# Kernel tuning notes

Measured on AMD Instinct MI355X. Metric: run time of the kernel, lower is better.

Reference implementation:

```python
import jax, jax.numpy as jnp
import numpy as np

EPS = 1e-6
NUM_SEMANTICS = 8
HIDDEN = 768
BATCH = 4096


def _gram_schmidt_single(vectors, fallback):
    """Sequential (classical, per-torch-code) Gram-Schmidt on (S, D) vectors.
    fallback: (S, D) random vectors used when a residual norm falls below EPS.
    """
    S = vectors.shape[0]
    qs = []
    for i in range(S):
        v = vectors[i]
        for j in range(i):
            qj = qs[j]
            denom = jnp.dot(qj, qj)
            safe_denom = jnp.where(denom > 0, denom, 1.0)
            proj = jnp.dot(v, qj) / safe_denom
            # torch: only subtract if ||q_j|| > eps
            v = jnp.where(jnp.sqrt(denom) > EPS, v - proj * qj, v)
        norm = jnp.linalg.norm(v)
        safe_norm = jnp.where(norm > 0, norm, 1.0)
        fb = fallback[i]
        fb = fb / jnp.linalg.norm(fb)
        q = jnp.where(norm > EPS, v / safe_norm, fb)
        qs.append(q)
    return jnp.stack(qs, axis=0)


def setup_inputs() -> dict:
    key = jax.random.key(0)
    semantic_reprs = jax.random.normal(key, (BATCH, NUM_SEMANTICS, HIDDEN), dtype=jnp.float32)
    return {"semantic_reprs": semantic_reprs}


def reference(semantic_reprs):
    B, S, D = semantic_reprs.shape
    # fixed fallback random vectors (stand-in for torch.randn_like in the degenerate branch)
    fallback = jax.random.normal(jax.random.key(42), (B, S, D), dtype=semantic_reprs.dtype)
    return jax.vmap(_gram_schmidt_single)(semantic_reprs, fallback)
```

## Files before the change

### kernel.cpp

```cpp
#include <hip/hip_runtime.h>


#define S_VECS 8
#define D_DIM 768
#define CHUNKS 192

typedef float f32x4 __attribute__((ext_vector_type(4)));

__device__ __forceinline__ float wave_reduce_sum(float x) {
#pragma unroll
    for (int off = 32; off >= 1; off >>= 1)
        x += __shfl_xor(x, off, 64);
    return x;
}

__global__ __launch_bounds__(192)
void gram_schmidt_kernel(const float* __restrict__ in, float* __restrict__ out) {
    const int wave = threadIdx.x >> 6;
    const int lane = threadIdx.x & 63;
    const int b = blockIdx.x;
    const int chunk = wave * 64 + lane;

    __shared__ float red[2][S_VECS][3];

    const int w1 = (wave == 2) ? 0 : wave + 1;
    const int w2 = (wave == 0) ? 2 : wave - 1;

    float v[S_VECS][4];
    const f32x4* src = reinterpret_cast<const f32x4*>(in) + (size_t)b * (S_VECS * CHUNKS);
#pragma unroll
    for (int s = 0; s < S_VECS; ++s) {
        f32x4 f = src[s * CHUNKS + chunk];
        v[s][0] = f.x; v[s][1] = f.y; v[s][2] = f.z; v[s][3] = f.w;
    }

    float inv_n[S_VECS];

#pragma unroll
    for (int i = 1; i < S_VECS; ++i) {
        const int p = i & 1;
        float d[S_VECS];
#pragma unroll
        for (int j = 0; j < S_VECS; ++j) {
            if (j < i) {
                float acc = 0.f;
#pragma unroll
                for (int e = 0; e < 4; ++e) acc += v[i][e] * v[j][e];
                d[j] = acc;
            }
        }
        float self = 0.f;
#pragma unroll
        for (int e = 0; e < 4; ++e) self += v[i - 1][e] * v[i - 1][e];

#pragma unroll
        for (int j = 0; j < S_VECS; ++j) {
            if (j < i) d[j] = wave_reduce_sum(d[j]);
        }
        self = wave_reduce_sum(self);

        if (lane == 0) {
#pragma unroll
            for (int j = 0; j < S_VECS; ++j) {
                if (j < i) red[p][j][wave] = d[j];
            }
            red[p][i][wave] = self;
        }
        __syncthreads();
#pragma unroll
        for (int j = 0; j < S_VECS; ++j) {
            if (j < i) d[j] += red[p][j][w1] + red[p][j][w2];
        }
        self += red[p][i][w1] + red[p][i][w2];
        inv_n[i - 1] = 1.0f / self;

#pragma unroll
        for (int j = 0; j < S_VECS; ++j) {
            if (j < i) {
                const float proj = d[j] * inv_n[j];
#pragma unroll
                for (int e = 0; e < 4; ++e) v[i][e] -= proj * v[j][e];
            }
        }
    }

    {
        float self = 0.f;
#pragma unroll
        for (int e = 0; e < 4; ++e) self += v[S_VECS - 1][e] * v[S_VECS - 1][e];
        self = wave_reduce_sum(self);
        if (lane == 0) red[0][0][wave] = self;
        __syncthreads();
        self += red[0][0][w1] + red[0][0][w2];
        inv_n[S_VECS - 1] = 1.0f / self;
    }

    f32x4* dst = reinterpret_cast<f32x4*>(out) + (size_t)b * (S_VECS * CHUNKS);
#pragma unroll
    for (int s = 0; s < S_VECS; ++s) {
        const float inv_norm = sqrtf(inv_n[s]);
        f32x4 f;
        f.x = v[s][0] * inv_norm;
        f.y = v[s][1] * inv_norm;
        f.z = v[s][2] * inv_norm;
        f.w = v[s][3] * inv_norm;
        __builtin_nontemporal_store(f, &dst[s * CHUNKS + chunk]);
    }
}

extern "C" void kernel_launch(void* const* d_in, const int* in_sizes, int n_in,
                              void* d_out, int out_size, void* d_ws, size_t ws_size,
                              hipStream_t stream) {
    const float* in = (const float*)d_in[0];
    float* out = (float*)d_out;
    const int B = in_sizes[0] / (S_VECS * D_DIM);
    gram_schmidt_kernel<<<B, 192, 0, stream>>>(in, out);
}
```

Before: 42.50 us.

## Replace sequential Gram-Schmidt with Gram matrix Cholesky and triangular inverse

Instead of projecting one vector at a time with a block barrier per step, the kernel computes the full 36-entry upper Gram matrix in one pass, reduces it across waves with a single barrier, and then runs a Cholesky factorisation redundantly in every thread. It inverts the triangular factor and forms the orthonormal outputs as linear combinations of the original vectors. This removes seven serialized reduce/sync rounds, in exchange for more wave shuffles at once, higher register pressure, and the numerical-stability and degenerate-case differences of Cholesky QR.

```diff
diff --git a/kernel.cpp b/kernel.cpp
--- a/kernel.cpp
+++ b/kernel.cpp
@@ -1,9 +1,9 @@
 #include <hip/hip_runtime.h>
 
 
-#define S_VECS 8
-#define D_DIM 768
+#define S 8
 #define CHUNKS 192
+#define IDX(i, j) ((i)*S - ((i) * ((i) + 1)) / 2 + (j))
 
 typedef float f32x4 __attribute__((ext_vector_type(4)));
 
@@ -15,95 +15,117 @@
 }
 
 __global__ __launch_bounds__(192)
-void gram_schmidt_kernel(const float* __restrict__ in, float* __restrict__ out) {
+void gs_chol_kernel(const float* __restrict__ in, float* __restrict__ out) {
     const int wave = threadIdx.x >> 6;
     const int lane = threadIdx.x & 63;
     const int b = blockIdx.x;
     const int chunk = wave * 64 + lane;
 
-    __shared__ float red[2][S_VECS][3];
+    __shared__ __align__(16) float red[3][36];
 
-    const int w1 = (wave == 2) ? 0 : wave + 1;
-    const int w2 = (wave == 0) ? 2 : wave - 1;
-
-    float v[S_VECS][4];
-    const f32x4* src = reinterpret_cast<const f32x4*>(in) + (size_t)b * (S_VECS * CHUNKS);
+    float v[S][4];
+    const f32x4* src = reinterpret_cast<const f32x4*>(in) + (size_t)b * (S * CHUNKS);
 #pragma unroll
-    for (int s = 0; s < S_VECS; ++s) {
+    for (int s = 0; s < S; ++s) {
         f32x4 f = src[s * CHUNKS + chunk];
         v[s][0] = f.x; v[s][1] = f.y; v[s][2] = f.z; v[s][3] = f.w;
     }
 
-    float inv_n[S_VECS];
-
+    float d[36];
 #pragma unroll
-    for (int i = 1; i < S_VECS; ++i) {
-        const int p = i & 1;
-        float d[S_VECS];
+    for (int i = 0; i < S; ++i) {
 #pragma unroll
-        for (int j = 0; j < S_VECS; ++j) {
-            if (j < i) {
+        for (int j = 0; j < S; ++j) {
+            if (j >= i) {
                 float acc = 0.f;
 #pragma unroll
                 for (int e = 0; e < 4; ++e) acc += v[i][e] * v[j][e];
-                d[j] = acc;
-            }
-        }
-        float self = 0.f;
-#pragma unroll
-        for (int e = 0; e < 4; ++e) self += v[i - 1][e] * v[i - 1][e];
-
-#pragma unroll
-        for (int j = 0; j < S_VECS; ++j) {
-            if (j < i) d[j] = wave_reduce_sum(d[j]);
-        }
-        self = wave_reduce_sum(self);
-
-        if (lane == 0) {
-#pragma unroll
-            for (int j = 0; j < S_VECS; ++j) {
-                if (j < i) red[p][j][wave] = d[j];
-            }
-            red[p][i][wave] = self;
-        }
-        __syncthreads();
-#pragma unroll
-        for (int j = 0; j < S_VECS; ++j) {
-            if (j < i) d[j] += red[p][j][w1] + red[p][j][w2];
-        }
-        self += red[p][i][w1] + red[p][i][w2];
-        inv_n[i - 1] = 1.0f / self;
-
-#pragma unroll
-        for (int j = 0; j < S_VECS; ++j) {
-            if (j < i) {
-                const float proj = d[j] * inv_n[j];
-#pragma unroll
-                for (int e = 0; e < 4; ++e) v[i][e] -= proj * v[j][e];
+                d[IDX(i, j)] = acc;
             }
         }
     }
 
-    {
-        float self = 0.f;
 #pragma unroll
-        for (int e = 0; e < 4; ++e) self += v[S_VECS - 1][e] * v[S_VECS - 1][e];
-        self = wave_reduce_sum(self);
-        if (lane == 0) red[0][0][wave] = self;
-        __syncthreads();
-        self += red[0][0][w1] + red[0][0][w2];
-        inv_n[S_VECS - 1] = 1.0f / self;
+    for (int t = 0; t < 36; ++t) d[t] = wave_reduce_sum(d[t]);
+
+    if (lane == 0) {
+#pragma unroll
+        for (int t = 0; t < 36; t += 4) {
+            f32x4 f;
+            f.x = d[t]; f.y = d[t + 1]; f.z = d[t + 2]; f.w = d[t + 3];
+            *reinterpret_cast<f32x4*>(&red[wave][t]) = f;
+        }
+    }
+    __syncthreads();
+
+    float G[36];
+#pragma unroll
+    for (int t = 0; t < 36; t += 4) {
+        f32x4 a = *reinterpret_cast<const f32x4*>(&red[0][t]);
+        f32x4 bb = *reinterpret_cast<const f32x4*>(&red[1][t]);
+        f32x4 c = *reinterpret_cast<const f32x4*>(&red[2][t]);
+        G[t]     = a.x + bb.x + c.x;
+        G[t + 1] = a.y + bb.y + c.y;
+        G[t + 2] = a.z + bb.z + c.z;
+        G[t + 3] = a.w + bb.w + c.w;
     }
 
-    f32x4* dst = reinterpret_cast<f32x4*>(out) + (size_t)b * (S_VECS * CHUNKS);
+    float invd[S];
 #pragma unroll
-    for (int s = 0; s < S_VECS; ++s) {
-        const float inv_norm = sqrtf(inv_n[s]);
+    for (int k = 0; k < S; ++k) {
+        float s0 = G[IDX(k, k)];
+#pragma unroll
+        for (int m = 0; m < S; ++m) {
+            if (m < k) { const float r = G[IDX(m, k)]; s0 -= r * r; }
+        }
+        const float inv = __frsqrt_rn(s0);
+        invd[k] = inv;
+        G[IDX(k, k)] = s0 * inv;
+#pragma unroll
+        for (int j = 0; j < S; ++j) {
+            if (j > k) {
+                float t = G[IDX(k, j)];
+#pragma unroll
+                for (int m = 0; m < S; ++m) {
+                    if (m < k) t -= G[IDX(m, k)] * G[IDX(m, j)];
+                }
+                G[IDX(k, j)] = t * inv;
+            }
+        }
+    }
+
+    float C[36];
+#pragma unroll
+    for (int s = 0; s < S; ++s) {
+        C[IDX(s, s)] = invd[s];
+#pragma unroll
+        for (int jj = 1; jj < S; ++jj) {
+            const int j = s - jj;
+            if (j >= 0) {
+                float t = 0.f;
+#pragma unroll
+                for (int m = 0; m < S; ++m) {
+                    if (m > j && m <= s) t += G[IDX(j, m)] * C[IDX(m, s)];
+                }
+                C[IDX(j, s)] = -t * invd[j];
+            }
+        }
+    }
+
+    f32x4* dst = reinterpret_cast<f32x4*>(out) + (size_t)b * (S * CHUNKS);
+#pragma unroll
+    for (int s = 0; s < S; ++s) {
+        float o0 = 0.f, o1 = 0.f, o2 = 0.f, o3 = 0.f;
+#pragma unroll
+        for (int j = 0; j < S; ++j) {
+            if (j <= s) {
+                const float c = C[IDX(j, s)];
+                o0 += c * v[j][0]; o1 += c * v[j][1];
+                o2 += c * v[j][2]; o3 += c * v[j][3];
+            }
+        }
         f32x4 f;
-        f.x = v[s][0] * inv_norm;
-        f.y = v[s][1] * inv_norm;
-        f.z = v[s][2] * inv_norm;
-        f.w = v[s][3] * inv_norm;
+        f.x = o0; f.y = o1; f.z = o2; f.w = o3;
         __builtin_nontemporal_store(f, &dst[s * CHUNKS + chunk]);
     }
 }
@@ -113,6 +135,6 @@
                               hipStream_t stream) {
     const float* in = (const float*)d_in[0];
     float* out = (float*)d_out;
-    const int B = in_sizes[0] / (S_VECS * D_DIM);
-    gram_schmidt_kernel<<<B, 192, 0, stream>>>(in, out);
+    const int B = in_sizes[0] / (S * 768);
+    gs_chol_kernel<<<B, 192, 0, stream>>>(in, out);
 }
```

Result: slower. 46.70 us (+9.9%).

## Process two batch items per block and use regular stores

Applied to the files above, without the earlier changes.

Each block now handles two batch items, issuing the global loads for both up front so the second item's loads overlap the first item's reductions and barriers. Grid size is halved. The nontemporal output store is also replaced with a normal store. The cost is roughly double the register footprint per thread, which can lower occupancy, and shared reduction buffers are reused across both items, which risks a race without an extra barrier.

```diff
diff --git a/kernel.cpp b/kernel.cpp
--- a/kernel.cpp
+++ b/kernel.cpp
@@ -14,26 +14,11 @@
     return x;
 }
 
-__global__ __launch_bounds__(192)
-void gram_schmidt_kernel(const float* __restrict__ in, float* __restrict__ out) {
-    const int wave = threadIdx.x >> 6;
-    const int lane = threadIdx.x & 63;
-    const int b = blockIdx.x;
-    const int chunk = wave * 64 + lane;
-
-    __shared__ float red[2][S_VECS][3];
-
-    const int w1 = (wave == 2) ? 0 : wave + 1;
-    const int w2 = (wave == 0) ? 2 : wave - 1;
-
-    float v[S_VECS][4];
-    const f32x4* src = reinterpret_cast<const f32x4*>(in) + (size_t)b * (S_VECS * CHUNKS);
-#pragma unroll
-    for (int s = 0; s < S_VECS; ++s) {
-        f32x4 f = src[s * CHUNKS + chunk];
-        v[s][0] = f.x; v[s][1] = f.y; v[s][2] = f.z; v[s][3] = f.w;
-    }
-
+__device__ __forceinline__ void process_store(float (&v)[S_VECS][4],
+                                              float (*red)[S_VECS][3],
+                                              int wave, int lane, int w1, int w2,
+                                              float* __restrict__ out,
+                                              size_t b, int chunk) {
     float inv_n[S_VECS];
 
 #pragma unroll
@@ -83,7 +68,6 @@
             }
         }
     }
-
     {
         float self = 0.f;
 #pragma unroll
@@ -95,7 +79,7 @@
         inv_n[S_VECS - 1] = 1.0f / self;
     }
 
-    f32x4* dst = reinterpret_cast<f32x4*>(out) + (size_t)b * (S_VECS * CHUNKS);
+    f32x4* dst = reinterpret_cast<f32x4*>(out) + b * (S_VECS * CHUNKS);
 #pragma unroll
     for (int s = 0; s < S_VECS; ++s) {
         const float inv_norm = sqrtf(inv_n[s]);
@@ -104,8 +88,39 @@
         f.y = v[s][1] * inv_norm;
         f.z = v[s][2] * inv_norm;
         f.w = v[s][3] * inv_norm;
-        __builtin_nontemporal_store(f, &dst[s * CHUNKS + chunk]);
+        dst[s * CHUNKS + chunk] = f;
     }
+}
+
+__global__ __launch_bounds__(192)
+void gram_schmidt_kernel(const float* __restrict__ in, float* __restrict__ out) {
+    const int wave = threadIdx.x >> 6;
+    const int lane = threadIdx.x & 63;
+    const int chunk = wave * 64 + lane;
+
+    __shared__ float red[2][S_VECS][3];
+    const int w1 = (wave == 2) ? 0 : wave + 1;
+    const int w2 = (wave == 0) ? 2 : wave - 1;
+
+    const size_t bA = (size_t)blockIdx.x * 2;
+    const size_t bB = bA + 1;
+
+    float vA[S_VECS][4], vB[S_VECS][4];
+    const f32x4* srcA = reinterpret_cast<const f32x4*>(in) + bA * (S_VECS * CHUNKS);
+    const f32x4* srcB = reinterpret_cast<const f32x4*>(in) + bB * (S_VECS * CHUNKS);
+#pragma unroll
+    for (int s = 0; s < S_VECS; ++s) {
+        f32x4 f = srcA[s * CHUNKS + chunk];
+        vA[s][0] = f.x; vA[s][1] = f.y; vA[s][2] = f.z; vA[s][3] = f.w;
+    }
+#pragma unroll
+    for (int s = 0; s < S_VECS; ++s) {
+        f32x4 f = srcB[s * CHUNKS + chunk];
+        vB[s][0] = f.x; vB[s][1] = f.y; vB[s][2] = f.z; vB[s][3] = f.w;
+    }
+
+    process_store(vA, red, wave, lane, w1, w2, out, bA, chunk);
+    process_store(vB, red, wave, lane, w1, w2, out, bB, chunk);
 }
 
 extern "C" void kernel_launch(void* const* d_in, const int* in_sizes, int n_in,
@@ -114,5 +129,5 @@
     const float* in = (const float*)d_in[0];
     float* out = (float*)d_out;
     const int B = in_sizes[0] / (S_VECS * D_DIM);
-    gram_schmidt_kernel<<<B, 192, 0, stream>>>(in, out);
+    gram_schmidt_kernel<<<B / 2, 192, 0, stream>>>(in, out);
 }
```

Result: slower. 49.55 us (+16.6%).
